# Performance work log

Hardware: AMD Instinct MI355X
Metric: run time of the kernel (lower is better)

Reference implementation:

```python
import jax, jax.numpy as jnp
import numpy as np

T, B, I, H = 512, 256, 120, 128
P = 1.5
D1, OUT = 512, 7


def _lstm_layer(x, W_ih, W_hh, b_ih, b_hh):
    # x: [T, B, F] -> outputs [T, B, H]; PyTorch gate order i, f, g, o
    xg = jnp.einsum('tbf,gf->tbg', x, W_ih) + b_ih + b_hh  # [T, B, 4H]
    Hh = W_hh.shape[1]

    def step(carry, xt):
        h, c = carry
        g = xt + h @ W_hh.T
        i, f, gg, o = jnp.split(g, 4, axis=-1)
        i = jax.nn.sigmoid(i)
        f = jax.nn.sigmoid(f)
        gg = jnp.tanh(gg)
        o = jax.nn.sigmoid(o)
        c = f * c + i * gg
        h = o * jnp.tanh(c)
        return (h, c), h

    h0 = jnp.zeros((x.shape[1], Hh), x.dtype)
    _, ys = jax.lax.scan(step, (h0, h0), xg)
    return ys


def setup_inputs() -> dict:
    key = jax.random.key(0)
    ks = jax.random.split(key, 14)
    s = lambda k, sh: (jax.random.normal(k, sh, jnp.float32) * 0.05)
    return {
        'input_seq': jax.random.normal(ks[0], (T, B, I), jnp.float32),
        'lens': jnp.sort(jax.random.randint(ks[1], (B,), 1, T + 1))[::-1],
        'W_ih0': s(ks[2], (4 * H, I)),
        'W_hh0': s(ks[3], (4 * H, H)),
        'b_ih0': s(ks[4], (4 * H,)),
        'b_hh0': s(ks[5], (4 * H,)),
        'W_ih1': s(ks[6], (4 * H, H)),
        'W_hh1': s(ks[7], (4 * H, H)),
        'b_ih1': s(ks[8], (4 * H,)),
        'b_hh1': s(ks[9], (4 * H,)),
        'W1': s(ks[10], (D1, H)),
        'b1': s(ks[11], (D1,)),
        'W2': s(ks[12], (OUT, D1)),
        'b2': s(ks[13], (OUT,)),
    }


def reference(input_seq, lens, W_ih0, W_hh0, b_ih0, b_hh0,
              W_ih1, W_hh1, b_ih1, b_hh1, W1, b1, W2, b2):
    h = _lstm_layer(input_seq, W_ih0, W_hh0, b_ih0, b_hh0)  # [T, B, H]
    h = _lstm_layer(h, W_ih1, W_hh1, b_ih1, b_hh1)          # [T, B, H]
    # pad_packed_sequence zeros positions >= len before the time-dim p-norm
    mask = (jnp.arange(T)[:, None] < lens[None, :])[..., None]  # [T, B, 1]
    h = jnp.where(mask, h, jnp.zeros((), h.dtype))
    pooled = jnp.sum(jnp.abs(h) ** P, axis=0) ** (1.0 / P)     # [B, H]
    pooled = pooled * (lens.astype(pooled.dtype) ** (-1.0 / P))[:, None]
    x = jax.nn.relu(pooled @ W1.T + b1)
    logits = x @ W2.T + b2
    return jax.nn.softmax(logits, axis=-1)
```

## Files before the change

### kernel.cpp

```cpp
#include <hip/hip_runtime.h>
#include <hip/hip_bf16.h>

#define TT 512
#define BB 256
#define II 120
#define HH 128
#define GG 512
#define D1 512
#define NOUT 7
#define TB (TT*BB)

typedef _Float16 f16x2 __attribute__((ext_vector_type(2)));
typedef _Float16 f16x4 __attribute__((ext_vector_type(4)));
typedef _Float16 f16x8 __attribute__((ext_vector_type(8)));
typedef float    f32x4 __attribute__((ext_vector_type(4)));

__device__ unsigned short g_xg[(size_t)TB * GG];
__device__ _Float16       g_h0[(size_t)TB * HH];
__device__ float          g_pooled[BB * HH];

__device__ inline float bf2f(unsigned short u) {
    return __uint_as_float(((unsigned)u) << 16);
}
__device__ inline unsigned short f2bf(float f) {
    unsigned u = __float_as_uint(f);
    return (unsigned short)((u + 0x7fffu + ((u >> 16) & 1u)) >> 16);
}
__device__ inline float fdot2(f16x2 a, f16x2 b, float c) {
#if __has_builtin(__builtin_amdgcn_fdot2)
    return __builtin_amdgcn_fdot2(a, b, c, false);
#else
    return c + (float)a[0] * (float)b[0] + (float)a[1] * (float)b[1];
#endif
}
__device__ inline float dpp_xor1(float v) {
#if __has_builtin(__builtin_amdgcn_mov_dpp)
    return __int_as_float(
        __builtin_amdgcn_mov_dpp(__float_as_int(v), 0xB1, 0xf, 0xf, true));
#else
    return __shfl_xor(v, 1, 4);
#endif
}

template <int LAYER>
__global__ __launch_bounds__(512) void gemm_mfma_kernel(
    const float* __restrict__ A0,
    const float* __restrict__ W,
    const float* __restrict__ bia,
    const float* __restrict__ bib)
{
    const int F  = (LAYER == 0) ? II : HH;
    const int m0 = blockIdx.x * 128;
    const int n0 = blockIdx.y * 128;
    const int t    = threadIdx.x;
    const int lane = t & 63;
    const int wv   = t >> 6;
    const int wm   = wv >> 2;
    const int wn   = wv & 3;
    const int l15  = lane & 15;
    const int lhi  = lane >> 4;

    __shared__ _Float16 As[128][40];
    __shared__ _Float16 Bs[128][40];

    f32x4 acc[4][2];
#pragma unroll
    for (int mi = 0; mi < 4; ++mi)
#pragma unroll
        for (int ni = 0; ni < 2; ++ni)
            acc[mi][ni] = f32x4{0.f, 0.f, 0.f, 0.f};

    const int srow = t >> 2;
    const int q    = t & 3;

#pragma unroll 1
    for (int kc = 0; kc < 4; ++kc) {
        const int k0 = kc * 32;
        if (LAYER == 0) {
#pragma unroll
            for (int h = 0; h < 2; ++h) {
                int k = k0 + q * 8 + h * 4;
                float4 v = make_float4(0.f, 0.f, 0.f, 0.f);
                if (k + 4 <= F) v = *(const float4*)&A0[(size_t)(m0 + srow) * II + k];
                f16x4 hv = {(_Float16)v.x, (_Float16)v.y, (_Float16)v.z, (_Float16)v.w};
                *(f16x4*)&As[srow][q * 8 + h * 4] = hv;
            }
        } else {
            int k = k0 + q * 8;
            f16x8 v = *(const f16x8*)&g_h0[(size_t)(m0 + srow) * HH + k];
            *(f16x8*)&As[srow][q * 8] = v;
        }
#pragma unroll
        for (int h = 0; h < 2; ++h) {
            int k = k0 + q * 8 + h * 4;
            float4 v = make_float4(0.f, 0.f, 0.f, 0.f);
            if (k + 4 <= F) v = *(const float4*)&W[(size_t)(n0 + srow) * F + k];
            f16x4 hv = {(_Float16)v.x, (_Float16)v.y, (_Float16)v.z, (_Float16)v.w};
            *(f16x4*)&Bs[srow][q * 8 + h * 4] = hv;
        }
        __syncthreads();

        f16x8 af[4], bf[2];
#pragma unroll
        for (int mi = 0; mi < 4; ++mi)
            af[mi] = *(const f16x8*)&As[wm * 64 + mi * 16 + l15][lhi * 8];
#pragma unroll
        for (int ni = 0; ni < 2; ++ni)
            bf[ni] = *(const f16x8*)&Bs[wn * 32 + ni * 16 + l15][lhi * 8];
#pragma unroll
        for (int mi = 0; mi < 4; ++mi)
#pragma unroll
            for (int ni = 0; ni < 2; ++ni)
                acc[mi][ni] = __builtin_amdgcn_mfma_f32_16x16x32_f16(
                    af[mi], bf[ni], acc[mi][ni], 0, 0, 0);
        __syncthreads();
    }

#pragma unroll
    for (int ni = 0; ni < 2; ++ni) {
        const int col = n0 + wn * 32 + ni * 16 + l15;
        const float bc = bia[col] + bib[col];
#pragma unroll
        for (int mi = 0; mi < 4; ++mi) {
#pragma unroll
            for (int j = 0; j < 4; ++j) {
                const int grow = m0 + wm * 64 + mi * 16 + lhi * 4 + j;
                g_xg[(size_t)grow * GG + col] = f2bf(acc[mi][ni][j] + bc);
            }
        }
    }
}

template <int LAYER>
__global__ __launch_bounds__(256) void lstm_kernel(
    const float* __restrict__ Whh,
    const int* __restrict__ lens)
{
    const int b = blockIdx.x;
    const int t = threadIdx.x;
    const int u = t >> 1;
    const int q = t & 1;
    const int r0 = q * 256 + u;
    const int r1 = r0 + 128;

    __shared__ __align__(16) _Float16 h_lds[2][HH];

    f16x2 w0[64], w1[64];
#pragma unroll
    for (int k4 = 0; k4 < 32; ++k4) {
        float4 v = *(const float4*)&Whh[(size_t)r0 * HH + k4 * 4];
        w0[k4 * 2 + 0] = f16x2{(_Float16)v.x, (_Float16)v.y};
        w0[k4 * 2 + 1] = f16x2{(_Float16)v.z, (_Float16)v.w};
        float4 v2 = *(const float4*)&Whh[(size_t)r1 * HH + k4 * 4];
        w1[k4 * 2 + 0] = f16x2{(_Float16)v2.x, (_Float16)v2.y};
        w1[k4 * 2 + 1] = f16x2{(_Float16)v2.z, (_Float16)v2.w};
    }
    if (t < HH) {
        h_lds[0][t] = (_Float16)0.f;
        h_lds[1][t] = (_Float16)0.f;
    }
    float c = 0.f, pool = 0.f;
    const int len = lens[b];
    __syncthreads();

    const unsigned short* xb = g_xg + (size_t)b * GG;
    const size_t xstride = (size_t)BB * GG;
    float x0 = bf2f(xb[r0]);
    float x1 = bf2f(xb[r1]);

    const float am = q ? 2.f : 1.f;
    const float as = q ? 2.f : 1.f;
    const float ao = q ? -1.f : 0.f;

    for (int step = 0; step < TT; ++step) {
        float nx0 = 0.f, nx1 = 0.f;
        if (step + 1 < TT) {
            const unsigned short* xn = xb + (size_t)(step + 1) * xstride;
            nx0 = bf2f(xn[r0]);
            nx1 = bf2f(xn[r1]);
        }
        const int rd = step & 1, wr = rd ^ 1;

        float a00 = 0.f, a01 = 0.f, a02 = 0.f, a03 = 0.f;
        float a10 = 0.f, a11 = 0.f, a12 = 0.f, a13 = 0.f;
#pragma unroll
        for (int seg = 0; seg < 8; ++seg) {
            f16x8 hv = *(const f16x8*)&h_lds[rd][seg * 8];
            f16x2 hA = {hv[0], hv[1]}, hB = {hv[2], hv[3]};
            f16x2 hC = {hv[4], hv[5]}, hD = {hv[6], hv[7]};
            a00 = fdot2(w0[seg * 4 + 0], hA, a00);
            a01 = fdot2(w0[seg * 4 + 1], hB, a01);
            a02 = fdot2(w0[seg * 4 + 2], hC, a02);
            a03 = fdot2(w0[seg * 4 + 3], hD, a03);
            a10 = fdot2(w1[seg * 4 + 0], hA, a10);
            a11 = fdot2(w1[seg * 4 + 1], hB, a11);
            a12 = fdot2(w1[seg * 4 + 2], hC, a12);
            a13 = fdot2(w1[seg * 4 + 3], hD, a13);
        }
        const float a0 = (a00 + a01) + (a02 + a03) + x0;
        const float a1 = (a10 + a11) + (a12 + a13) + x1;

        const float s0 = 1.f / (1.f + __expf(-(a0 * am)));
        const float act0 = s0 * as + ao;
        const float act1 = 1.f / (1.f + __expf(-a1));

        const float p0 = dpp_xor1(act0);
        const float p1 = dpp_xor1(act1);
        const float i_ = q ? p0 : act0;
        const float f_ = q ? p1 : act1;
        const float g_ = q ? act0 : p0;
        const float o_ = q ? act1 : p1;

        c = f_ * c + i_ * g_;
        const float e2 = __expf(-2.f * c);
        const float th = 2.f / (1.f + e2) - 1.f;
        const float hv2 = o_ * th;

        if (LAYER == 0) {
            if (q) g_h0[((size_t)step * BB + b) * HH + u] = (_Float16)hv2;
        } else {
            if (step < len) {
                const float ah = fabsf(hv2);
                pool += ah * sqrtf(ah);
            }
        }
        if (!q) h_lds[wr][u] = (_Float16)hv2;
        __syncthreads();
        x0 = nx0;
        x1 = nx1;
    }

    if (LAYER == 1 && !q) {
        const float s = powf(pool, 2.f / 3.f) * powf((float)len, -2.f / 3.f);
        g_pooled[b * HH + u] = s;
    }
}

__global__ __launch_bounds__(512) void mlp_kernel(
    const float* __restrict__ W1, const float* __restrict__ b1,
    const float* __restrict__ W2, const float* __restrict__ b2,
    float* __restrict__ out)
{
    const int b = blockIdx.x;
    const int t = threadIdx.x;
    __shared__ __align__(16) float pl[HH];
    __shared__ float x1[D1];
    __shared__ float lg[NOUT];

    if (t < HH) pl[t] = g_pooled[b * HH + t];
    __syncthreads();

    float acc = b1[t];
#pragma unroll
    for (int k4 = 0; k4 < 32; ++k4) {
        float4 wv = *(const float4*)&W1[(size_t)t * HH + k4 * 4];
        float4 pv = *(const float4*)&pl[k4 * 4];
        acc += wv.x * pv.x + wv.y * pv.y + wv.z * pv.z + wv.w * pv.w;
    }
    x1[t] = fmaxf(acc, 0.f);
    __syncthreads();

    if (t < NOUT) {
        float a = b2[t];
        for (int d = 0; d < D1; ++d) a += x1[d] * W2[(size_t)t * D1 + d];
        lg[t] = a;
    }
    __syncthreads();
    if (t < NOUT) {
        float m = lg[0];
#pragma unroll
        for (int j = 1; j < NOUT; ++j) m = fmaxf(m, lg[j]);
        float s = 0.f;
#pragma unroll
        for (int j = 0; j < NOUT; ++j) s += __expf(lg[j] - m);
        out[b * NOUT + t] = __expf(lg[t] - m) / s;
    }
}

extern "C" void kernel_launch(void* const* d_in, const int* in_sizes, int n_in,
                              void* d_out, int out_size, void* d_ws, size_t ws_size,
                              hipStream_t stream)
{
    const float* x      = (const float*)d_in[0];
    const int*   lens   = (const int*)d_in[1];
    const float* W_ih0  = (const float*)d_in[2];
    const float* W_hh0  = (const float*)d_in[3];
    const float* b_ih0  = (const float*)d_in[4];
    const float* b_hh0  = (const float*)d_in[5];
    const float* W_ih1  = (const float*)d_in[6];
    const float* W_hh1  = (const float*)d_in[7];
    const float* b_ih1  = (const float*)d_in[8];
    const float* b_hh1  = (const float*)d_in[9];
    const float* W1     = (const float*)d_in[10];
    const float* b1     = (const float*)d_in[11];
    const float* W2     = (const float*)d_in[12];
    const float* b2     = (const float*)d_in[13];
    float* out = (float*)d_out;

    dim3 gg(TB / 128, GG / 128);
    gemm_mfma_kernel<0><<<gg, 512, 0, stream>>>(x, W_ih0, b_ih0, b_hh0);
    lstm_kernel<0><<<BB, 256, 0, stream>>>(W_hh0, lens);
    gemm_mfma_kernel<1><<<gg, 512, 0, stream>>>(x, W_ih1, b_ih1, b_hh1);
    lstm_kernel<1><<<BB, 256, 0, stream>>>(W_hh1, lens);
    mlp_kernel<<<BB, 512, 0, stream>>>(W1, b1, W2, b2, out);
}
```

Before: 672.7 us.

## Process two batch rows per LSTM block to reuse register-resident weights

Each LSTM recurrence block now handles two batch elements and reuses the W_hh weights held in registers for both, halving the grid to 128 blocks. The goal is to amortise the per-step barrier and LDS latency over twice the work and to cut the redundant weight loads. In exchange each step's critical path roughly doubles in arithmetic, and with only 128 blocks on a machine with more CUs, part of the GPU may sit idle. Register pressure also rises.

```diff
diff --git a/kernel.cpp b/kernel.cpp
--- a/kernel.cpp
+++ b/kernel.cpp
@@ -136,14 +136,15 @@
     const float* __restrict__ Whh,
     const int* __restrict__ lens)
 {
-    const int b = blockIdx.x;
+    const int b0 = blockIdx.x * 2;
+    const int b1 = b0 + 1;
     const int t = threadIdx.x;
     const int u = t >> 1;
     const int q = t & 1;
     const int r0 = q * 256 + u;
     const int r1 = r0 + 128;
 
-    __shared__ __align__(16) _Float16 h_lds[2][HH];
+    __shared__ __align__(16) _Float16 h_lds[2][2][HH];
 
     f16x2 w0[64], w1[64];
 #pragma unroll
@@ -156,83 +157,123 @@
         w1[k4 * 2 + 1] = f16x2{(_Float16)v2.z, (_Float16)v2.w};
     }
     if (t < HH) {
-        h_lds[0][t] = (_Float16)0.f;
-        h_lds[1][t] = (_Float16)0.f;
-    }
-    float c = 0.f, pool = 0.f;
-    const int len = lens[b];
+        h_lds[0][0][t] = (_Float16)0.f; h_lds[0][1][t] = (_Float16)0.f;
+        h_lds[1][0][t] = (_Float16)0.f; h_lds[1][1][t] = (_Float16)0.f;
+    }
+    float cA = 0.f, cB = 0.f, poolA = 0.f, poolB = 0.f;
+    const int lenA = lens[b0];
+    const int lenB = lens[b1];
     __syncthreads();
 
-    const unsigned short* xb = g_xg + (size_t)b * GG;
+    const unsigned short* xa = g_xg + (size_t)b0 * GG;
+    const unsigned short* xb = g_xg + (size_t)b1 * GG;
     const size_t xstride = (size_t)BB * GG;
-    float x0 = bf2f(xb[r0]);
-    float x1 = bf2f(xb[r1]);
+    float xA0 = bf2f(xa[r0]), xA1 = bf2f(xa[r1]);
+    float xB0 = bf2f(xb[r0]), xB1 = bf2f(xb[r1]);
 
     const float am = q ? 2.f : 1.f;
     const float as = q ? 2.f : 1.f;
     const float ao = q ? -1.f : 0.f;
 
     for (int step = 0; step < TT; ++step) {
-        float nx0 = 0.f, nx1 = 0.f;
+        float nA0 = 0.f, nA1 = 0.f, nB0 = 0.f, nB1 = 0.f;
         if (step + 1 < TT) {
-            const unsigned short* xn = xb + (size_t)(step + 1) * xstride;
-            nx0 = bf2f(xn[r0]);
-            nx1 = bf2f(xn[r1]);
+            const unsigned short* xna = xa + (size_t)(step + 1) * xstride;
+            const unsigned short* xnb = xb + (size_t)(step + 1) * xstride;
+            nA0 = bf2f(xna[r0]); nA1 = bf2f(xna[r1]);
+            nB0 = bf2f(xnb[r0]); nB1 = bf2f(xnb[r1]);
         }
         const int rd = step & 1, wr = rd ^ 1;
 
-        float a00 = 0.f, a01 = 0.f, a02 = 0.f, a03 = 0.f;
-        float a10 = 0.f, a11 = 0.f, a12 = 0.f, a13 = 0.f;
+        float aA00 = 0.f, aA01 = 0.f, aA02 = 0.f, aA03 = 0.f;
+        float aA10 = 0.f, aA11 = 0.f, aA12 = 0.f, aA13 = 0.f;
 #pragma unroll
         for (int seg = 0; seg < 8; ++seg) {
-            f16x8 hv = *(const f16x8*)&h_lds[rd][seg * 8];
+            f16x8 hv = *(const f16x8*)&h_lds[0][rd][seg * 8];
             f16x2 hA = {hv[0], hv[1]}, hB = {hv[2], hv[3]};
             f16x2 hC = {hv[4], hv[5]}, hD = {hv[6], hv[7]};
-            a00 = fdot2(w0[seg * 4 + 0], hA, a00);
-            a01 = fdot2(w0[seg * 4 + 1], hB, a01);
-            a02 = fdot2(w0[seg * 4 + 2], hC, a02);
-            a03 = fdot2(w0[seg * 4 + 3], hD, a03);
-            a10 = fdot2(w1[seg * 4 + 0], hA, a10);
-            a11 = fdot2(w1[seg * 4 + 1], hB, a11);
-            a12 = fdot2(w1[seg * 4 + 2], hC, a12);
-            a13 = fdot2(w1[seg * 4 + 3], hD, a13);
-        }
-        const float a0 = (a00 + a01) + (a02 + a03) + x0;
-        const float a1 = (a10 + a11) + (a12 + a13) + x1;
-
-        const float s0 = 1.f / (1.f + __expf(-(a0 * am)));
-        const float act0 = s0 * as + ao;
-        const float act1 = 1.f / (1.f + __expf(-a1));
-
-        const float p0 = dpp_xor1(act0);
-        const float p1 = dpp_xor1(act1);
-        const float i_ = q ? p0 : act0;
-        const float f_ = q ? p1 : act1;
-        const float g_ = q ? act0 : p0;
-        const float o_ = q ? act1 : p1;
-
-        c = f_ * c + i_ * g_;
-        const float e2 = __expf(-2.f * c);
-        const float th = 2.f / (1.f + e2) - 1.f;
-        const float hv2 = o_ * th;
+            aA00 = fdot2(w0[seg * 4 + 0], hA, aA00);
+            aA01 = fdot2(w0[seg * 4 + 1], hB, aA01);
+            aA02 = fdot2(w0[seg * 4 + 2], hC, aA02);
+            aA03 = fdot2(w0[seg * 4 + 3], hD, aA03);
+            aA10 = fdot2(w1[seg * 4 + 0], hA, aA10);
+            aA11 = fdot2(w1[seg * 4 + 1], hB, aA11);
+            aA12 = fdot2(w1[seg * 4 + 2], hC, aA12);
+            aA13 = fdot2(w1[seg * 4 + 3], hD, aA13);
+        }
+        float aB00 = 0.f, aB01 = 0.f, aB02 = 0.f, aB03 = 0.f;
+        float aB10 = 0.f, aB11 = 0.f, aB12 = 0.f, aB13 = 0.f;
+#pragma unroll
+        for (int seg = 0; seg < 8; ++seg) {
+            f16x8 hv = *(const f16x8*)&h_lds[1][rd][seg * 8];
+            f16x2 hA = {hv[0], hv[1]}, hB = {hv[2], hv[3]};
+            f16x2 hC = {hv[4], hv[5]}, hD = {hv[6], hv[7]};
+            aB00 = fdot2(w0[seg * 4 + 0], hA, aB00);
+            aB01 = fdot2(w0[seg * 4 + 1], hB, aB01);
+            aB02 = fdot2(w0[seg * 4 + 2], hC, aB02);
+            aB03 = fdot2(w0[seg * 4 + 3], hD, aB03);
+            aB10 = fdot2(w1[seg * 4 + 0], hA, aB10);
+            aB11 = fdot2(w1[seg * 4 + 1], hB, aB11);
+            aB12 = fdot2(w1[seg * 4 + 2], hC, aB12);
+            aB13 = fdot2(w1[seg * 4 + 3], hD, aB13);
+        }
+
+        const float aA0 = (aA00 + aA01) + (aA02 + aA03) + xA0;
+        const float aA1 = (aA10 + aA11) + (aA12 + aA13) + xA1;
+        const float sA0 = 1.f / (1.f + __expf(-(aA0 * am)));
+        const float actA0 = sA0 * as + ao;
+        const float actA1 = 1.f / (1.f + __expf(-aA1));
+        const float pA0 = dpp_xor1(actA0);
+        const float pA1 = dpp_xor1(actA1);
+        const float iA = q ? pA0 : actA0;
+        const float fA = q ? pA1 : actA1;
+        const float gA = q ? actA0 : pA0;
+        const float oA = q ? actA1 : pA1;
+        cA = fA * cA + iA * gA;
+        const float thA = 2.f / (1.f + __expf(-2.f * cA)) - 1.f;
+        const float hvA = oA * thA;
+
+        const float aB0 = (aB00 + aB01) + (aB02 + aB03) + xB0;
+        const float aB1 = (aB10 + aB11) + (aB12 + aB13) + xB1;
+        const float sB0 = 1.f / (1.f + __expf(-(aB0 * am)));
+        const float actB0 = sB0 * as + ao;
+        const float actB1 = 1.f / (1.f + __expf(-aB1));
+        const float pB0 = dpp_xor1(actB0);
+        const float pB1 = dpp_xor1(actB1);
+        const float iB = q ? pB0 : actB0;
+        const float fB = q ? pB1 : actB1;
+        const float gB = q ? actB0 : pB0;
+        const float oB = q ? actB1 : pB1;
+        cB = fB * cB + iB * gB;
+        const float thB = 2.f / (1.f + __expf(-2.f * cB)) - 1.f;
+        const float hvB = oB * thB;
 
         if (LAYER == 0) {
-            if (q) g_h0[((size_t)step * BB + b) * HH + u] = (_Float16)hv2;
+            if (q) {
+                g_h0[((size_t)step * BB + b0) * HH + u] = (_Float16)hvA;
+                g_h0[((size_t)step * BB + b1) * HH + u] = (_Float16)hvB;
+            }
         } else {
-            if (step < len) {
-                const float ah = fabsf(hv2);
-                pool += ah * sqrtf(ah);
-            }
-        }
-        if (!q) h_lds[wr][u] = (_Float16)hv2;
+            if (step < lenA) {
+                const float ah = fabsf(hvA);
+                poolA += ah * sqrtf(ah);
+            }
+            if (step < lenB) {
+                const float ah = fabsf(hvB);
+                poolB += ah * sqrtf(ah);
+            }
+        }
+        if (!q) {
+            h_lds[0][wr][u] = (_Float16)hvA;
+            h_lds[1][wr][u] = (_Float16)hvB;
+        }
         __syncthreads();
-        x0 = nx0;
-        x1 = nx1;
+        xA0 = nA0; xA1 = nA1; xB0 = nB0; xB1 = nB1;
     }
 
     if (LAYER == 1 && !q) {
-        const float s = powf(pool, 2.f / 3.f) * powf((float)len, -2.f / 3.f);
-        g_pooled[b * HH + u] = s;
+        g_pooled[b0 * HH + u] = powf(poolA, 2.f / 3.f) * powf((float)lenA, -2.f / 3.f);
+        g_pooled[b1 * HH + u] = powf(poolB, 2.f / 3.f) * powf((float)lenB, -2.f / 3.f);
     }
 }
 
@@ -299,8 +340,8 @@
 
     dim3 gg(TB / 128, GG / 128);
     gemm_mfma_kernel<0><<<gg, 512, 0, stream>>>(x, W_ih0, b_ih0, b_hh0);
-    lstm_kernel<0><<<BB, 256, 0, stream>>>(W_hh0, lens);
+    lstm_kernel<0><<<BB / 2, 256, 0, stream>>>(W_hh0, lens);
     gemm_mfma_kernel<1><<<gg, 512, 0, stream>>>(x, W_ih1, b_ih1, b_hh1);
-    lstm_kernel<1><<<BB, 256, 0, stream>>>(W_hh1, lens);
+    lstm_kernel<1><<<BB / 2, 256, 0, stream>>>(W_hh1, lens);
     mlp_kernel<<<BB, 512, 0, stream>>>(W1, b1, W2, b2, out);
 }
```

Measured after the change: 949.6 us. 1.41x slower.
